# Kernel optimization log

Measured on AMD Instinct MI355X. Metric: run time of the kernel, lower is better.

The kernel has to match this reference:

```python
import jax, jax.numpy as jnp
from jax import lax
import numpy as np

L = 1024   # latent_size
R = 128    # latent_size // k
G = 2      # groups
KS = 2     # kernel_size
BI, BT, T, TXT = 32, 128, 64, 300
EPS = 1e-5


def setup_inputs() -> dict:
    key = jax.random.key(0)
    ks = jax.random.split(key, 24)
    n = lambda i, shape, s=0.05: jax.random.normal(ks[i], shape, jnp.float32) * s
    return {
        "img_embed": jax.random.normal(ks[0], (BI, 36, L), jnp.float32),
        "cap_embed": jax.random.normal(ks[1], (BT, T, TXT), jnp.float32),
        # reduce_img / reduce_txt (1x1 conv == linear over channels)
        "W_ri": n(2, (R, L)), "b_ri": n(3, (R,)),
        "W_rt": n(4, (R, TXT)), "b_rt": n(5, (R,)),
        # two MixedConv blocks stacked on a leading axis of size 2
        "mk_W": n(6, (2, R * R * KS // G, R)), "mk_b": n(7, (2, R * R * KS // G)),  # hypernet kernel Linear
        "mbias_W": n(8, (2, R, R)), "mbias_b": n(9, (2, R)),                        # hypernet bias Linear
        "wn_g": 1.0 + n(10, (2, R), 0.1), "wn_b": n(11, (2, R), 0.1),               # BN over generated kernel
        "ca_W": n(12, (2, R, R // G, KS)), "ca_b": n(13, (2, R)),                   # static grouped conv1a
        "bn_g": 1.0 + n(14, (2, 2 * R), 0.1), "bn_b": n(15, (2, 2 * R), 0.1),       # BN on cat activations
        "c1_W": n(16, (2, R, 2 * R)), "c1_b": n(17, (2, R)),                        # 1x1 mixing conv
        # txt_fc 1x1 conv
        "W_fc": n(18, (L, R)), "b_fc": n(19, (L,)),
    }


def _bn(x, g, b):
    # training-mode BatchNorm1d over (N, C, L): stats per channel over (N, L)
    m = x.mean(axis=(0, 2), keepdims=True)
    v = x.var(axis=(0, 2), keepdims=True)
    return g[None, :, None] * (x - m) * lax.rsqrt(v + EPS) + b[None, :, None]


def _gconv(x, w):
    # grouped valid conv1d, x: (B, Cin, T), w: (Cout, Cin//G, KS)
    return lax.conv_general_dilated(x, w, (1,), 'VALID',
                                    feature_group_count=G,
                                    dimension_numbers=('NCH', 'OIH', 'NCH'))


def _l2norm(x, axis=-1):
    return x / jnp.linalg.norm(x, axis=axis, keepdims=True)


def reference(img_embed, cap_embed, W_ri, b_ri, W_rt, b_rt, mk_W, mk_b,
              mbias_W, mbias_b, wn_g, wn_b, ca_W, ca_b, bn_g, bn_b,
              c1_W, c1_b, W_fc, b_fc):
    imgs = img_embed.transpose(0, 2, 1)   # (BI, L, 36)
    caps = cap_embed.transpose(0, 2, 1)   # (BT, 300, T)
    img_global = imgs.mean(-1)            # (BI, L)
    cap_red = jnp.einsum('oc,bct->bot', W_rt, caps) + b_rt[None, :, None]  # (BT, R, T)
    img_red = jnp.einsum('oc,bct->bot', W_ri, imgs) + b_ri[None, :, None]  # (BI, R, 36)
    img_vec = img_red.mean(-1)            # (BI, R) hypernet conditioning

    def mixed(x, base, j):
        # hypernet-generated grouped conv kernel + bias
        kern = (mk_W[j] @ base + mk_b[j]).reshape(R, R // G, KS)  # (out, in//g, ks)
        kern = _bn(kern.transpose(1, 0, 2), wn_g[j], wn_b[j]).transpose(1, 0, 2)
        bias = mbias_W[j] @ base + mbias_b[j]                     # (R,)
        px = _gconv(x, kern) + bias[None, :, None]
        ax = _gconv(x, ca_W[j]) + ca_b[j][None, :, None]
        h = jnp.concatenate([px, ax], axis=1)                     # (BT, 2R, T')
        h = jax.nn.relu(_bn(h, bn_g[j], bn_b[j]))
        return jnp.einsum('oc,bct->bot', c1_W[j], h) + c1_b[j][None, :, None]

    def per_image(base, img_g):
        x = mixed(cap_red, base, 0)
        x = mixed(x, base, 1)
        x = jnp.einsum('oc,bct->bot', W_fc, x) + b_fc[None, :, None]  # (BT, L, T-2)
        tv = _l2norm(jnp.max(x, axis=-1), axis=-1)                    # (BT, L)
        iv = _l2norm(img_g, axis=-1)                                  # (L,)
        return tv @ iv                                                # (BT,)

    sims = jax.vmap(per_image)(img_vec, img_global)  # (BI, BT)
    return sims
```

## Files before the change

### kernel.cpp

```cpp
#include <hip/hip_runtime.h>


#define EPSc 1e-5f
typedef unsigned short u16;
typedef __bf16 bf16x8 __attribute__((ext_vector_type(8)));
typedef float f32x4 __attribute__((ext_vector_type(4)));

static const long OFF_IMG_GLOBAL = 0;
static const long OFF_IV         = 32768;
static const long OFF_IMG_VEC    = 65536;
static const long OFF_CAP_RED    = 69632;
static const long OFF_KERN       = 1118208;
static const long OFF_KERN_BF    = 2166784;
static const long OFF_CA_BF      = 2691072;
static const long OFF_C1W0       = 2707456;
static const long OFF_C1W1       = 2715648;
static const long OFF_WFC        = 2732032;
static const long OFF_CAP_BF     = 2797568;
static const long OFF_SHARED1    = 3330112;
static const long OFF_ST_AX0     = 4378688;
static const long FIXED_END      = 4378944;

__device__ inline u16 f2bf(float f) {
  union { float f; unsigned u; } v; v.f = f;
  unsigned u = v.u;
  return (u16)((u + 0x7FFFu + ((u >> 16) & 1u)) >> 16);
}
__device__ inline float bf2f(u16 u) {
  union { unsigned u; float f; } v; v.u = ((unsigned)u) << 16; return v.f;
}

__global__ void k_img(const float* __restrict__ img, float* __restrict__ img_global,
                      float* __restrict__ iv) {
  int b = blockIdx.x, tid = threadIdx.x;
  __shared__ float gl[1024];
  __shared__ float red[256];
  float ssq = 0.f;
  for (int l = tid; l < 1024; l += 256) {
    float s = 0.f;
    for (int p = 0; p < 36; ++p) s += img[((long)b*36 + p)*1024 + l];
    float g = s * (1.f/36.f);
    gl[l] = g;
    img_global[(long)b*1024 + l] = g;
    ssq += g*g;
  }
  red[tid] = ssq;
  __syncthreads();
  for (int off = 128; off > 0; off >>= 1) {
    if (tid < off) red[tid] += red[tid+off];
    __syncthreads();
  }
  float inv = rsqrtf(red[0]);
  for (int l = tid; l < 1024; l += 256) iv[(long)b*1024 + l] = gl[l]*inv;
}

__global__ void k_imgvec(const float* __restrict__ img_global, const float* __restrict__ W_ri,
                         const float* __restrict__ b_ri, float* __restrict__ img_vec) {
  int b = blockIdx.x, tid = threadIdx.x;
  __shared__ float gl[1024];
  for (int l = tid; l < 1024; l += 128) gl[l] = img_global[(long)b*1024 + l];
  __syncthreads();
  const float* w = W_ri + (long)tid*1024;
  float acc = b_ri[tid];
  for (int l = 0; l < 1024; l += 4) {
    float4 wv = *(const float4*)(w + l);
    float4 gv = *(const float4*)(gl + l);
    acc += wv.x*gv.x + wv.y*gv.y + wv.z*gv.z + wv.w*gv.w;
  }
  img_vec[(long)b*128 + tid] = acc;
}

__global__ void k_capred(const float* __restrict__ cap, const float* __restrict__ W_rt,
                         const float* __restrict__ b_rt, float* __restrict__ cap_red) {
  int tg = blockIdx.x, b = blockIdx.y, tid = threadIdx.x;
  __shared__ float xs[300*16];
  for (int idx = tid; idx < 16*300; idx += 128) {
    int q = idx / 300, c = idx - q*300;
    xs[c*16 + q] = cap[((long)b*64 + tg*16 + q)*300 + c];
  }
  __syncthreads();
  int o = tid;
  const float* w = W_rt + (long)o*300;
  float acc[16];
  float bb = b_rt[o];
  #pragma unroll
  for (int q = 0; q < 16; ++q) acc[q] = bb;
  for (int c = 0; c < 300; ++c) {
    float wv = w[c];
    const float* xp = &xs[c*16];
    float4 x0 = *(const float4*)(xp);
    float4 x1 = *(const float4*)(xp+4);
    float4 x2 = *(const float4*)(xp+8);
    float4 x3 = *(const float4*)(xp+12);
    acc[0]+=wv*x0.x; acc[1]+=wv*x0.y; acc[2]+=wv*x0.z; acc[3]+=wv*x0.w;
    acc[4]+=wv*x1.x; acc[5]+=wv*x1.y; acc[6]+=wv*x1.z; acc[7]+=wv*x1.w;
    acc[8]+=wv*x2.x; acc[9]+=wv*x2.y; acc[10]+=wv*x2.z; acc[11]+=wv*x2.w;
    acc[12]+=wv*x3.x; acc[13]+=wv*x3.y; acc[14]+=wv*x3.z; acc[15]+=wv*x3.w;
  }
  float* outp = cap_red + ((long)b*128 + o)*64 + tg*16;
  #pragma unroll
  for (int q = 0; q < 16; ++q) outp[q] = acc[q];
}

__global__ void k_cap2bf(const float* __restrict__ cap_red, u16* __restrict__ cap_bf) {
  int b = blockIdx.x, tid = threadIdx.x;
  __shared__ float ls[128*64];
  for (int idx = tid; idx < 8192; idx += 256) ls[idx] = cap_red[(long)b*8192 + idx];
  __syncthreads();
  for (int idx = tid; idx < 65*128; idx += 256) {
    int t = idx >> 7, c = idx & 127;
    float v = (t < 64) ? ls[c*64 + t] : 0.f;
    cap_bf[((long)b*65 + t)*128 + c] = f2bf(v);
  }
}

__global__ void k_kerngen(const float* __restrict__ mk_W, const float* __restrict__ mk_b,
                          const float* __restrict__ img_vec, float* __restrict__ kern) {
  int j = blockIdx.x >> 7, kb = blockIdx.x & 127, tid = threadIdx.x;
  int k = kb*128 + tid;
  __shared__ float bl[128*32];
  for (int idx = tid; idx < 4096; idx += 128) {
    int i = idx >> 7, r = idx & 127;
    bl[r*32 + i] = img_vec[idx];
  }
  __syncthreads();
  const float* wrow = mk_W + ((long)j*16384 + k)*128;
  float acc[32];
  #pragma unroll
  for (int i = 0; i < 32; ++i) acc[i] = 0.f;
  for (int r = 0; r < 128; ++r) {
    float w = wrow[r];
    const float* bp = &bl[r*32];
    #pragma unroll
    for (int i = 0; i < 32; ++i) acc[i] += w * bp[i];
  }
  float kb_ = mk_b[(long)j*16384 + k];
  for (int i = 0; i < 32; ++i)
    kern[((long)j*32 + i)*16384 + k] = acc[i] + kb_;
}

__global__ void k_kernbn(const float* __restrict__ kern, const float* __restrict__ wn_g,
                         const float* __restrict__ wn_b, u16* __restrict__ kbf) {
  int j = blockIdx.x >> 5, i = blockIdx.x & 31, o = threadIdx.x;
  const float* row = kern + ((long)((j*32+i)*128 + o))*128;
  float s = 0.f, q = 0.f;
  for (int c = 0; c < 128; ++c) { float v = row[c]; s += v; q += v*v; }
  float mean = s * (1.f/128.f);
  float var = q * (1.f/128.f) - mean*mean;
  float rstd = rsqrtf(var + EPSc);
  float sc = wn_g[j*128+o] * rstd;
  float sh = wn_b[j*128+o] - mean*sc;
  int g = o >> 6, op = o & 63;
  u16* base = kbf + (((long)(j*32+i)*2 + g)*2)*4096 + op*64;
  for (int c = 0; c < 128; ++c) {
    float v = row[c]*sc + sh;
    int kp = c & 1, cp = c >> 1;
    base[(long)kp*4096 + cp] = f2bf(v);
  }
}

__global__ void k_ca2bf(const float* __restrict__ caW, u16* __restrict__ cabf) {
  int idx = blockIdx.x*256 + threadIdx.x;
  int j = idx >> 14, r = idx & 16383;
  int o = r >> 7, ck = r & 127, cp = ck >> 1, kp = ck & 1;
  int g = o >> 6, op = o & 63;
  cabf[(((long)(j*2+g)*2 + kp))*4096 + op*64 + cp] = f2bf(caW[idx]);
}

__global__ void k_c1bf(const float* __restrict__ c1W, u16* __restrict__ w0, u16* __restrict__ w1) {
  int idx = blockIdx.x*256 + threadIdx.x;
  if (idx < 16384) { int o = idx >> 7, c = idx & 127; w0[idx] = f2bf(c1W[o*256 + c]); }
  else { int e = idx - 16384; w1[e] = f2bf(c1W[32768 + e]); }
}

__global__ void k_wfc2bf(const float* __restrict__ W, u16* __restrict__ out) {
  int idx = (blockIdx.x*256 + threadIdx.x)*4;
  float4 v = *(const float4*)(W + idx);
  u16 o[4] = { f2bf(v.x), f2bf(v.y), f2bf(v.z), f2bf(v.w) };
  *(uint2*)(out + idx) = *(const uint2*)(o);
}

__global__ void k_conv(const float* __restrict__ X, long xstr, int Tin, int Tout,
                       const float* __restrict__ Wt, long wstr,
                       const float* __restrict__ bias, int bstr,
                       float* __restrict__ Y, long ystr) {
  int b = blockIdx.x, ic = blockIdx.y, tid = threadIdx.x;
  __shared__ float xls[128*64];
  const float* Xb = X + (long)ic*xstr + (long)b*128*Tin;
  for (int idx = tid; idx < 128*Tin; idx += 256) {
    int c = idx / Tin, t = idx - c*Tin;
    xls[c*64 + t] = Xb[idx];
  }
  __syncthreads();
  int oi = tid & 63, tq = tid >> 6;
  int o0 = oi*2, g = o0 >> 6, t0 = tq*16;
  const float* wa = Wt + (long)ic*wstr + (long)o0*128;
  const float* wb = wa + 128;
  float acc0[16], acc1[16];
  #pragma unroll
  for (int tt = 0; tt < 16; ++tt) { acc0[tt] = 0.f; acc1[tt] = 0.f; }
  bool f16ok = (t0 + 16 < Tin);
  for (int cp = 0; cp < 64; ++cp) {
    float wa0 = wa[cp*2], wa1 = wa[cp*2+1];
    float wb0 = wb[cp*2], wb1 = wb[cp*2+1];
    const float* row = &xls[(g*64 + cp)*64 + t0];
    float f[17];
    float4 v0 = *(const float4*)(row);
    float4 v1 = *(const float4*)(row+4);
    float4 v2 = *(const float4*)(row+8);
    float4 v3 = *(const float4*)(row+12);
    f[0]=v0.x; f[1]=v0.y; f[2]=v0.z; f[3]=v0.w;
    f[4]=v1.x; f[5]=v1.y; f[6]=v1.z; f[7]=v1.w;
    f[8]=v2.x; f[9]=v2.y; f[10]=v2.z; f[11]=v2.w;
    f[12]=v3.x; f[13]=v3.y; f[14]=v3.z; f[15]=v3.w;
    f[16] = f16ok ? row[16] : 0.f;
    #pragma unroll
    for (int tt = 0; tt < 16; ++tt) {
      acc0[tt] += wa0*f[tt] + wa1*f[tt+1];
      acc1[tt] += wb0*f[tt] + wb1*f[tt+1];
    }
  }
  float bb0 = bias[ic*bstr + o0], bb1 = bias[ic*bstr + o0 + 1];
  float* y0 = Y + (long)ic*ystr + ((long)b*128 + o0)*Tout;
  float* y1 = y0 + Tout;
  #pragma unroll
  for (int tt = 0; tt < 16; ++tt) {
    int t = t0 + tt;
    if (t < Tout) { y0[t] = acc0[tt] + bb0; y1[t] = acc1[tt] + bb1; }
  }
}

__global__ void k_stats(const float* __restrict__ X, long xstr, int Tlen,
                        const float* __restrict__ gp, const float* __restrict__ bp,
                        float* __restrict__ st, int sstr) {
  int c = blockIdx.x, ic = blockIdx.y, tid = threadIdx.x;
  __shared__ float r1[256], r2[256];
  const float* base = X + (long)ic*xstr + (long)c*Tlen;
  int n = 128*Tlen;
  float s = 0.f, q = 0.f;
  for (int idx = tid; idx < n; idx += 256) {
    int b = idx / Tlen, t = idx - b*Tlen;
    float v = base[(long)b*128*Tlen + t];
    s += v; q += v*v;
  }
  r1[tid] = s; r2[tid] = q;
  __syncthreads();
  for (int off = 128; off > 0; off >>= 1) {
    if (tid < off) { r1[tid] += r1[tid+off]; r2[tid] += r2[tid+off]; }
    __syncthreads();
  }
  if (tid == 0) {
    float mean = r1[0] / n;
    float var = r2[0] / n - mean*mean;
    float rstd = rsqrtf(var + EPSc);
    float sc = gp[c]*rstd;
    st[(long)ic*sstr + c] = sc;
    st[(long)ic*sstr + 128 + c] = bp[c] - mean*sc;
  }
}

__global__ void k_mix_shared(const float* __restrict__ X1, const float* __restrict__ st,
                             const float* __restrict__ W, float* __restrict__ Y) {
  int b = blockIdx.x, tid = threadIdx.x;
  __shared__ float xs[128*64];
  __shared__ float ssc[128], ssh[128];
  int o4 = (tid & 31)*4, t0 = (tid >> 5)*8;
  float acc[4][8];
  #pragma unroll
  for (int r = 0; r < 4; ++r)
    #pragma unroll
    for (int tt = 0; tt < 8; ++tt) acc[r][tt] = 0.f;
  if (tid < 128) { ssc[tid] = st[tid]; ssh[tid] = st[128+tid]; }
  __syncthreads();
  const float* Xb = X1 + (long)b*128*63;
  for (int idx = tid; idx < 128*63; idx += 256) {
    int c = idx / 63, t = idx - c*63;
    xs[c*64 + t] = fmaxf(Xb[idx]*ssc[c] + ssh[c], 0.f);
  }
  __syncthreads();
  for (int c = 0; c < 128; ++c) {
    float4 f0 = *(const float4*)&xs[c*64 + t0];
    float4 f1 = *(const float4*)&xs[c*64 + t0 + 4];
    #pragma unroll
    for (int r = 0; r < 4; ++r) {
      float w = W[(long)(o4+r)*256 + 128 + c];
      acc[r][0] += w*f0.x; acc[r][1] += w*f0.y; acc[r][2] += w*f0.z; acc[r][3] += w*f0.w;
      acc[r][4] += w*f1.x; acc[r][5] += w*f1.y; acc[r][6] += w*f1.z; acc[r][7] += w*f1.w;
    }
  }
  #pragma unroll
  for (int r = 0; r < 4; ++r)
    #pragma unroll
    for (int tt = 0; tt < 8; ++tt) {
      int t = t0 + tt;
      if (t < 63) Y[((long)b*64 + t)*128 + o4 + r] = acc[r][tt];
    }
}

__global__ __launch_bounds__(256) void k_conv_mfma2(
    const u16* __restrict__ X, long x_img_str, int tr_stride,
    const u16* __restrict__ kernA, const u16* __restrict__ statA,
    int tvalid, u16* __restrict__ H, int ctot, float* __restrict__ part) {
  int bc = blockIdx.x, v = blockIdx.y, i = blockIdx.z;
  int tid = threadIdx.x, w = tid >> 6, lane = tid & 63;
  int l15 = lane & 15, l4 = lane >> 4;
  int g = v & 1;
  const u16* A = (v >= 2) ? (statA + (long)g*8192)
                          : (kernA + (long)i*16384 + (long)g*8192);
  __shared__ u16 xls[65*64];
  bf16x8 af[2][2];
  #pragma unroll
  for (int kp = 0; kp < 2; ++kp)
    #pragma unroll
    for (int ks = 0; ks < 2; ++ks)
      af[kp][ks] = *(const bf16x8*)(A + ((long)(kp*64 + w*16 + l15))*64 + ks*32 + l4*8);
  int cbase = v*64 + w*16;
  float s[4] = {0.f,0.f,0.f,0.f}, q[4] = {0.f,0.f,0.f,0.f};
  for (int bb = 0; bb < 4; ++bb) {
    int b = bc*4 + bb;
    const u16* src = X + x_img_str*i + ((long)b*tr_stride)*128 + g*64;
    __syncthreads();
    for (int idx = tid; idx < 65*8; idx += 256) {
      int r = idx >> 3, ch = idx & 7;
      uint4 d = *(const uint4*)(src + (long)r*128 + ch*8);
      *(uint4*)(xls + r*64 + ((ch ^ (r & 7))*8)) = d;
    }
    __syncthreads();
    #pragma unroll
    for (int nt = 0; nt < 4; ++nt) {
      f32x4 acc = {0.f,0.f,0.f,0.f};
      #pragma unroll
      for (int kp = 0; kp < 2; ++kp) {
        int row = nt*16 + l15 + kp;
        #pragma unroll
        for (int ks = 0; ks < 2; ++ks) {
          int ch = (ks*4 + l4) ^ (row & 7);
          bf16x8 bf = *(const bf16x8*)(xls + row*64 + ch*8);
          acc = __builtin_amdgcn_mfma_f32_16x16x32_bf16(af[kp][ks], bf, acc, 0, 0, 0);
        }
      }
      int t = nt*16 + l15;
      u16 h4[4] = { f2bf(acc[0]), f2bf(acc[1]), f2bf(acc[2]), f2bf(acc[3]) };
      *(uint2*)(H + ((long)((i*128 + b)*64 + t))*ctot + cbase + l4*4) = *(const uint2*)(h4);
      float m = (t < tvalid) ? 1.f : 0.f;
      #pragma unroll
      for (int r = 0; r < 4; ++r) {
        float vv = acc[r]*m;
        s[r] += vv; q[r] += vv*vv;
      }
    }
  }
  #pragma unroll
  for (int r = 0; r < 4; ++r) {
    #pragma unroll
    for (int mk = 1; mk < 16; mk <<= 1) {
      s[r] += __shfl_xor(s[r], mk);
      q[r] += __shfl_xor(q[r], mk);
    }
  }
  if (l15 == 0) {
    #pragma unroll
    for (int r = 0; r < 4; ++r) {
      int c = cbase + l4*4 + r;
      long base = ((long)i*ctot + c)*64;
      part[base + bc] = s[r];
      part[base + 32 + bc] = q[r];
    }
  }
}

__global__ void k_finstats2(const float* __restrict__ part, float* __restrict__ scsh,
                            const float* __restrict__ g, const float* __restrict__ bta,
                            int ct, float n, int total) {
  int idx = blockIdx.x*256 + threadIdx.x;
  if (idx >= total) return;
  int c = idx & (ct - 1);
  const float* p = part + (long)idx*64;
  float s = 0.f, q = 0.f;
  #pragma unroll
  for (int k = 0; k < 32; ++k) { s += p[k]; q += p[32+k]; }
  float mean = s / n, var = q / n - mean*mean;
  float sc = g[c] * rsqrtf(var + EPSc);
  scsh[idx*2] = sc;
  scsh[idx*2 + 1] = bta[c] - mean*sc;
}

template<int CK>
__global__ __launch_bounds__(256) void k_mix_mfma2(
    const u16* __restrict__ X, const u16* __restrict__ A,
    const float* __restrict__ scsh,
    const float* __restrict__ c1b, const float* __restrict__ addbuf,
    u16* __restrict__ Q, int tvalid) {
  constexpr int NCH = CK/8;
  constexpr int KST = CK/32;
  int bc = blockIdx.x, m = blockIdx.y, i = blockIdx.z;
  int tid = threadIdx.x, w = tid >> 6, lane = tid & 63;
  int l15 = lane & 15, l4 = lane >> 4;
  __shared__ u16 xls[64*CK];
  __shared__ float lsc[CK], lsh[CK];
  for (int c = tid; c < CK; c += 256) {
    lsc[c] = scsh[((long)i*CK + c)*2];
    lsh[c] = scsh[((long)i*CK + c)*2 + 1];
  }
  int oa = m*64 + w*16 + l15;
  bf16x8 af[KST];
  #pragma unroll
  for (int ks = 0; ks < KST; ++ks)
    af[ks] = *(const bf16x8*)(A + (long)oa*CK + ks*32 + l4*8);
  int ob = m*64 + w*16 + l4*4;
  float4 cb;
  cb.x = c1b[ob]; cb.y = c1b[ob+1]; cb.z = c1b[ob+2]; cb.w = c1b[ob+3];
  for (int bb = 0; bb < 4; ++bb) {
    int b = bc*4 + bb;
    const u16* src = X + ((long)(i*128 + b)*64)*CK;
    __syncthreads();
    for (int idx = tid; idx < 64*NCH; idx += 256) {
      int r = idx / NCH, ch = idx & (NCH - 1);
      uint4 d = *(const uint4*)(src + (long)r*CK + ch*8);
      unsigned dd[4] = {d.x, d.y, d.z, d.w};
      int c0 = ch*8;
      u16 o[8];
      #pragma unroll
      for (int pi = 0; pi < 4; ++pi) {
        float v0 = bf2f((u16)(dd[pi] & 0xFFFF));
        float v1 = bf2f((u16)(dd[pi] >> 16));
        v0 = fmaxf(v0*lsc[c0 + pi*2] + lsh[c0 + pi*2], 0.f);
        v1 = fmaxf(v1*lsc[c0 + pi*2 + 1] + lsh[c0 + pi*2 + 1], 0.f);
        o[pi*2] = f2bf(v0); o[pi*2 + 1] = f2bf(v1);
      }
      *(uint4*)(xls + r*CK + (((ch ^ (r & 15)) & (NCH - 1))*8)) = *(const uint4*)o;
    }
    __syncthreads();
    #pragma unroll
    for (int nt = 0; nt < 4; ++nt) {
      f32x4 acc = {0.f,0.f,0.f,0.f};
      int row = nt*16 + l15;
      #pragma unroll
      for (int ks = 0; ks < KST; ++ks) {
        int ch = ((ks*4 + l4) ^ (row & 15)) & (NCH - 1);
        bf16x8 bf = *(const bf16x8*)(xls + row*CK + ch*8);
        acc = __builtin_amdgcn_mfma_f32_16x16x32_bf16(af[ks], bf, acc, 0, 0, 0);
      }
      int t = row;
      if (t < tvalid) {
        float4 ad = {0.f,0.f,0.f,0.f};
        if (addbuf) ad = *(const float4*)(addbuf + ((long)b*64 + t)*128 + ob);
        u16 h4[4] = { f2bf(acc[0] + cb.x + ad.x), f2bf(acc[1] + cb.y + ad.y),
                      f2bf(acc[2] + cb.z + ad.z), f2bf(acc[3] + cb.w + ad.w) };
        *(uint2*)(Q + ((long)((i*128 + b)*64 + t))*128 + ob) = *(const uint2*)(h4);
      }
    }
  }
}

__global__ __launch_bounds__(256) void k_fc3(
    const u16* __restrict__ Qt, const u16* __restrict__ Wb,
    const float* __restrict__ bfc, const float* __restrict__ ivp,
    float* __restrict__ pp) {
  int bg = blockIdx.x, sl = blockIdx.y, i = blockIdx.z;
  int tid = threadIdx.x, w = tid >> 6, lane = tid & 63;
  int l15 = lane & 15, l4 = lane >> 4;
  int lbase = sl*256 + w*64;
  bf16x8 wf[4][4];
  #pragma unroll
  for (int lt = 0; lt < 4; ++lt)
    #pragma unroll
    for (int ks = 0; ks < 4; ++ks)
      wf[lt][ks] = *(const bf16x8*)(Wb + (long)(lbase + lt*16 + l15)*128 + ks*32 + l4*8);
  float bfr[4], ivr[4];
  const float* ivb = ivp + (long)i*1024;
  #pragma unroll
  for (int lt = 0; lt < 4; ++lt) {
    bfr[lt] = bfc[lbase + lt*16 + l15];
    ivr[lt] = ivb[lbase + lt*16 + l15];
  }
  __shared__ float red[4][2];
  float en = (l4 == 0) ? 1.f : 0.f;
  for (int bb = 0; bb < 8; ++bb) {
    int b = bg*8 + bb;
    const u16* Qb = Qt + ((long)(i*128 + b))*64*128;
    float mx[4] = {-3e38f, -3e38f, -3e38f, -3e38f};
    #pragma unroll
    for (int nt = 0; nt < 4; ++nt) {
      bf16x8 qf[4];
      #pragma unroll
      for (int ks = 0; ks < 4; ++ks)
        qf[ks] = *(const bf16x8*)(Qb + (nt*16 + l15)*128 + ks*32 + l4*8);
      #pragma unroll
      for (int lt = 0; lt < 4; ++lt) {
        f32x4 acc = {0.f,0.f,0.f,0.f};
        acc = __builtin_amdgcn_mfma_f32_16x16x32_bf16(qf[0], wf[lt][0], acc, 0,0,0);
        acc = __builtin_amdgcn_mfma_f32_16x16x32_bf16(qf[1], wf[lt][1], acc, 0,0,0);
        acc = __builtin_amdgcn_mfma_f32_16x16x32_bf16(qf[2], wf[lt][2], acc, 0,0,0);
        acc = __builtin_amdgcn_mfma_f32_16x16x32_bf16(qf[3], wf[lt][3], acc, 0,0,0);
        float m01 = fmaxf(acc[0], acc[1]);
        float m23 = fmaxf(acc[2], acc[3]);
        if (nt == 3 && l4 == 3) m23 = -3e38f;
        mx[lt] = fmaxf(mx[lt], fmaxf(m01, m23));
      }
    }
    float ssc = 0.f, ddc = 0.f;
    #pragma unroll
    for (int lt = 0; lt < 4; ++lt) {
      float m = mx[lt];
      m = fmaxf(m, __shfl_xor(m, 16));
      m = fmaxf(m, __shfl_xor(m, 32));
      float tv = m + bfr[lt];
      ssc += en*tv*tv;
      ddc += en*tv*ivr[lt];
    }
    #pragma unroll
    for (int mk = 1; mk < 16; mk <<= 1) { ssc += __shfl_xor(ssc, mk); ddc += __shfl_xor(ddc, mk); }
    if (lane == 0) { red[w][0] = ssc; red[w][1] = ddc; }
    __syncthreads();
    if (tid == 0) {
      float S = red[0][0] + red[1][0] + red[2][0] + red[3][0];
      float D = red[0][1] + red[1][1] + red[2][1] + red[3][1];
      long o = (((long)i*128 + b)*4 + sl)*2;
      pp[o] = S; pp[o+1] = D;
    }
    __syncthreads();
  }
}

__global__ void k_fcred(const float* __restrict__ pp, float* __restrict__ outp) {
  int i = blockIdx.x, b = threadIdx.x;
  const float* p = pp + (((long)i*128 + b)*4)*2;
  float S = p[0] + p[2] + p[4] + p[6];
  float D = p[1] + p[3] + p[5] + p[7];
  outp[i*128 + b] = D * rsqrtf(S);
}

extern "C" void kernel_launch(void* const* d_in, const int* in_sizes, int n_in,
                              void* d_out, int out_size, void* d_ws, size_t ws_size,
                              hipStream_t stream) {
  (void)in_sizes; (void)n_in; (void)out_size;
  const float* img_embed = (const float*)d_in[0];
  const float* cap_embed = (const float*)d_in[1];
  const float* W_ri  = (const float*)d_in[2];
  const float* b_ri  = (const float*)d_in[3];
  const float* W_rt  = (const float*)d_in[4];
  const float* b_rt  = (const float*)d_in[5];
  const float* mk_W  = (const float*)d_in[6];
  const float* mk_b  = (const float*)d_in[7];
  const float* wn_g  = (const float*)d_in[10];
  const float* wn_b  = (const float*)d_in[11];
  const float* ca_W  = (const float*)d_in[12];
  const float* ca_b  = (const float*)d_in[13];
  const float* bn_g  = (const float*)d_in[14];
  const float* bn_b  = (const float*)d_in[15];
  const float* c1_W  = (const float*)d_in[16];
  const float* c1_b  = (const float*)d_in[17];
  const float* W_fc  = (const float*)d_in[18];
  const float* b_fc  = (const float*)d_in[19];
  float* out = (float*)d_out;
  float* ws  = (float*)d_ws;

  float* img_global = ws + OFF_IMG_GLOBAL;
  float* iv       = ws + OFF_IV;
  float* img_vec  = ws + OFF_IMG_VEC;
  float* cap_red  = ws + OFF_CAP_RED;
  float* kern     = ws + OFF_KERN;
  u16*   kern_bf  = (u16*)(ws + OFF_KERN_BF);
  u16*   ca_bf    = (u16*)(ws + OFF_CA_BF);
  u16*   c1w0     = (u16*)(ws + OFF_C1W0);
  u16*   c1w1     = (u16*)(ws + OFF_C1W1);
  u16*   wfcb     = (u16*)(ws + OFF_WFC);
  u16*   cap_bf   = (u16*)(ws + OFF_CAP_BF);
  float* shared1  = ws + OFF_SHARED1;
  float* st_ax0   = ws + OFF_ST_AX0;

  int NC = 4;
  {
    auto need = [](long nc) -> size_t { return (size_t)(FIXED_END + nc*2621440L + 128) * 4u; };
    if (ws_size >= need(32)) NC = 32;
    else if (ws_size >= need(16)) NC = 16;
    else if (ws_size >= need(8)) NC = 8;
  }

  float* part  = ws + OFF_KERN;
  float* scsh0 = ws + OFF_KERN + 524288;
  float* scsh1 = ws + OFF_KERN + 524288 + 8192;
  float* pp    = ws + OFF_KERN + 524288 + 8192 + 16384;

  long base = FIXED_END;
  float* ax0f = ws + base;
  u16* P0 = (u16*)(ws + base);
  u16* Q0 = (u16*)(ws + base + (long)NC*524288);
  u16* H1 = (u16*)(ws + base + (long)NC*524288*2 + 64);
  u16* Q1 = (u16*)(ws + base + (long)NC*524288*2 + 64 + (long)NC*1048576);

  k_img<<<32, 256, 0, stream>>>(img_embed, img_global, iv);
  k_imgvec<<<32, 128, 0, stream>>>(img_global, W_ri, b_ri, img_vec);
  k_capred<<<dim3(4,128), 128, 0, stream>>>(cap_embed, W_rt, b_rt, cap_red);
  k_cap2bf<<<128, 256, 0, stream>>>(cap_red, cap_bf);
  k_kerngen<<<256, 128, 0, stream>>>(mk_W, mk_b, img_vec, kern);
  k_kernbn<<<64, 128, 0, stream>>>(kern, wn_g, wn_b, kern_bf);
  k_ca2bf<<<128, 256, 0, stream>>>(ca_W, ca_bf);
  k_c1bf<<<192, 256, 0, stream>>>(c1_W, c1w0, c1w1);
  k_wfc2bf<<<128, 256, 0, stream>>>(W_fc, wfcb);

  k_conv<<<dim3(128,1), 256, 0, stream>>>(cap_red, 0, 64, 63, ca_W, 0, ca_b, 0, ax0f, 0);
  k_stats<<<dim3(128,1), 256, 0, stream>>>(ax0f, 0, 63, bn_g+128, bn_b+128, st_ax0, 0);
  k_mix_shared<<<128, 256, 0, stream>>>(ax0f, st_ax0, c1_W, shared1);

  for (int ch = 0; ch < 32/NC; ++ch) {
    int i0 = ch*NC;
    k_conv_mfma2<<<dim3(32,2,NC), 256, 0, stream>>>(
        cap_bf, 0L, 65, kern_bf + (long)i0*16384, ca_bf, 63, P0, 128, part);
    k_finstats2<<<dim3((NC*128+255)/256), 256, 0, stream>>>(
        part, scsh0, bn_g, bn_b, 128, 8064.f, NC*128);
    k_mix_mfma2<128><<<dim3(32,2,NC), 256, 0, stream>>>(
        P0, c1w0, scsh0, c1_b, shared1, Q0, 63);
    k_conv_mfma2<<<dim3(32,4,NC), 256, 0, stream>>>(
        Q0, 1048576L, 64, kern_bf + (long)(32 + i0)*16384, ca_bf + 16384, 62, H1, 256, part);
    k_finstats2<<<dim3((NC*256+255)/256), 256, 0, stream>>>(
        part, scsh1, bn_g + 256, bn_b + 256, 256, 7936.f, NC*256);
    k_mix_mfma2<256><<<dim3(32,2,NC), 256, 0, stream>>>(
        H1, c1w1, scsh1, c1_b + 128, nullptr, Q1, 62);
    k_fc3<<<dim3(16,4,NC), 256, 0, stream>>>(
        Q1, wfcb, b_fc, iv + (long)i0*1024, pp);
    k_fcred<<<NC, 128, 0, stream>>>(pp, out + i0*128);
  }
}
```

Baseline: 649.6 us.

## Software-pipeline global loads in conv, mix and fc kernels with register prefetch

The conv and mix MFMA kernels now prefetch the next batch's tile into registers while computing the current one, then write it to shared memory after a barrier, so global latency overlaps with MFMA work. The fc kernel double-buffers Q fragments across four captions per block, doubling the grid. It drops the block-level shared reduction in favour of per-wave partial outputs, and the final reduction kernel now sums 16 partials instead of 4. The cost is higher register pressure from the staged tiles and fragments, and more partial-sum traffic.

Measured after the change: 717.9 us. 1.11x slower.

```diff
diff --git a/kernel.cpp b/kernel.cpp
--- a/kernel.cpp
+++ b/kernel.cpp
@@ -297,7 +297,7 @@
     }
 }
 
-__global__ __launch_bounds__(256) void k_conv_mfma2(
+__global__ __launch_bounds__(256) void k_conv_mfma3(
     const u16* __restrict__ X, long x_img_str, int tr_stride,
     const u16* __restrict__ kernA, const u16* __restrict__ statA,
     int tvalid, u16* __restrict__ H, int ctot, float* __restrict__ part) {
@@ -316,16 +316,27 @@
       af[kp][ks] = *(const bf16x8*)(A + ((long)(kp*64 + w*16 + l15))*64 + ks*32 + l4*8);
   int cbase = v*64 + w*16;
   float s[4] = {0.f,0.f,0.f,0.f}, q[4] = {0.f,0.f,0.f,0.f};
+  uint4 s0, s1, s2;
+  int r0 = tid >> 3, ch0 = tid & 7;
+  int r1 = (tid + 256) >> 3, ch1 = tid & 7;
+  auto loadX = [&](int b) {
+    const u16* src = X + x_img_str*i + ((long)b*tr_stride)*128 + g*64;
+    s0 = *(const uint4*)(src + (long)r0*128 + ch0*8);
+    s1 = *(const uint4*)(src + (long)r1*128 + ch1*8);
+    if (tid < 8) s2 = *(const uint4*)(src + 64L*128 + tid*8);
+  };
+  auto writeX = [&]() {
+    *(uint4*)(xls + r0*64 + ((ch0 ^ (r0 & 7))*8)) = s0;
+    *(uint4*)(xls + r1*64 + ((ch1 ^ (r1 & 7))*8)) = s1;
+    if (tid < 8) *(uint4*)(xls + 64*64 + tid*8) = s2;
+  };
+  loadX(bc*4);
+  writeX();
+  __syncthreads();
+  #pragma unroll
   for (int bb = 0; bb < 4; ++bb) {
     int b = bc*4 + bb;
-    const u16* src = X + x_img_str*i + ((long)b*tr_stride)*128 + g*64;
-    __syncthreads();
-    for (int idx = tid; idx < 65*8; idx += 256) {
-      int r = idx >> 3, ch = idx & 7;
-      uint4 d = *(const uint4*)(src + (long)r*128 + ch*8);
-      *(uint4*)(xls + r*64 + ((ch ^ (r & 7))*8)) = d;
-    }
-    __syncthreads();
+    if (bb < 3) loadX(b + 1);
     #pragma unroll
     for (int nt = 0; nt < 4; ++nt) {
       f32x4 acc = {0.f,0.f,0.f,0.f};
@@ -349,6 +360,8 @@
         s[r] += vv; q[r] += vv*vv;
       }
     }
+    __syncthreads();
+    if (bb < 3) { writeX(); __syncthreads(); }
   }
   #pragma unroll
   for (int r = 0; r < 4; ++r) {
@@ -386,13 +399,14 @@
 }
 
 template<int CK>
-__global__ __launch_bounds__(256) void k_mix_mfma2(
+__global__ __launch_bounds__(256) void k_mix_mfma3(
     const u16* __restrict__ X, const u16* __restrict__ A,
     const float* __restrict__ scsh,
     const float* __restrict__ c1b, const float* __restrict__ addbuf,
     u16* __restrict__ Q, int tvalid) {
   constexpr int NCH = CK/8;
   constexpr int KST = CK/32;
+  constexpr int NST = (64*NCH)/256;
   int bc = blockIdx.x, m = blockIdx.y, i = blockIdx.z;
   int tid = threadIdx.x, w = tid >> 6, lane = tid & 63;
   int l15 = lane & 15, l4 = lane >> 4;
@@ -410,14 +424,21 @@
   int ob = m*64 + w*16 + l4*4;
   float4 cb;
   cb.x = c1b[ob]; cb.y = c1b[ob+1]; cb.z = c1b[ob+2]; cb.w = c1b[ob+3];
-  for (int bb = 0; bb < 4; ++bb) {
-    int b = bc*4 + bb;
+  uint4 st[NST];
+  auto loadX = [&](int b) {
     const u16* src = X + ((long)(i*128 + b)*64)*CK;
-    __syncthreads();
-    for (int idx = tid; idx < 64*NCH; idx += 256) {
+    #pragma unroll
+    for (int k = 0; k < NST; ++k) {
+      int idx = tid + k*256;
+      st[k] = *(const uint4*)(src + (long)(idx/NCH)*CK + (idx & (NCH-1))*8);
+    }
+  };
+  auto writeX = [&]() {
+    #pragma unroll
+    for (int k = 0; k < NST; ++k) {
+      int idx = tid + k*256;
       int r = idx / NCH, ch = idx & (NCH - 1);
-      uint4 d = *(const uint4*)(src + (long)r*CK + ch*8);
-      unsigned dd[4] = {d.x, d.y, d.z, d.w};
+      unsigned dd[4] = {st[k].x, st[k].y, st[k].z, st[k].w};
       int c0 = ch*8;
       u16 o[8];
       #pragma unroll
@@ -430,7 +451,15 @@
       }
       *(uint4*)(xls + r*CK + (((ch ^ (r & 15)) & (NCH - 1))*8)) = *(const uint4*)o;
     }
-    __syncthreads();
+  };
+  loadX(bc*4);
+  __syncthreads();
+  writeX();
+  __syncthreads();
+  #pragma unroll
+  for (int bb = 0; bb < 4; ++bb) {
+    int b = bc*4 + bb;
+    if (bb < 3) loadX(b + 1);
     #pragma unroll
     for (int nt = 0; nt < 4; ++nt) {
       f32x4 acc = {0.f,0.f,0.f,0.f};
@@ -450,10 +479,12 @@
         *(uint2*)(Q + ((long)((i*128 + b)*64 + t))*128 + ob) = *(const uint2*)(h4);
       }
     }
-  }
-}
-
-__global__ __launch_bounds__(256) void k_fc3(
+    __syncthreads();
+    if (bb < 3) { writeX(); __syncthreads(); }
+  }
+}
+
+__global__ __launch_bounds__(256) void k_fc4(
     const u16* __restrict__ Qt, const u16* __restrict__ Wb,
     const float* __restrict__ bfc, const float* __restrict__ ivp,
     float* __restrict__ pp) {
@@ -474,25 +505,26 @@
     bfr[lt] = bfc[lbase + lt*16 + l15];
     ivr[lt] = ivb[lbase + lt*16 + l15];
   }
-  __shared__ float red[4][2];
-  float en = (l4 == 0) ? 1.f : 0.f;
-  for (int bb = 0; bb < 8; ++bb) {
-    int b = bg*8 + bb;
-    const u16* Qb = Qt + ((long)(i*128 + b))*64*128;
-    float mx[4] = {-3e38f, -3e38f, -3e38f, -3e38f};
-    #pragma unroll
-    for (int nt = 0; nt < 4; ++nt) {
-      bf16x8 qf[4];
+  bf16x8 qA[4][4], qB[4][4];
+  auto loadQ = [&](bf16x8 (&qf)[4][4], int b) {
+    const u16* Qb = Qt + ((long)(i*128 + b))*8192;
+    #pragma unroll
+    for (int nt = 0; nt < 4; ++nt)
       #pragma unroll
       for (int ks = 0; ks < 4; ++ks)
-        qf[ks] = *(const bf16x8*)(Qb + (nt*16 + l15)*128 + ks*32 + l4*8);
+        qf[nt][ks] = *(const bf16x8*)(Qb + (nt*16 + l15)*128 + ks*32 + l4*8);
+  };
+  auto computeQ = [&](bf16x8 (&qf)[4][4], int b) {
+    float mx[4] = {-3e38f, -3e38f, -3e38f, -3e38f};
+    #pragma unroll
+    for (int nt = 0; nt < 4; ++nt) {
       #pragma unroll
       for (int lt = 0; lt < 4; ++lt) {
         f32x4 acc = {0.f,0.f,0.f,0.f};
-        acc = __builtin_amdgcn_mfma_f32_16x16x32_bf16(qf[0], wf[lt][0], acc, 0,0,0);
-        acc = __builtin_amdgcn_mfma_f32_16x16x32_bf16(qf[1], wf[lt][1], acc, 0,0,0);
-        acc = __builtin_amdgcn_mfma_f32_16x16x32_bf16(qf[2], wf[lt][2], acc, 0,0,0);
-        acc = __builtin_amdgcn_mfma_f32_16x16x32_bf16(qf[3], wf[lt][3], acc, 0,0,0);
+        acc = __builtin_amdgcn_mfma_f32_16x16x32_bf16(qf[nt][0], wf[lt][0], acc, 0,0,0);
+        acc = __builtin_amdgcn_mfma_f32_16x16x32_bf16(qf[nt][1], wf[lt][1], acc, 0,0,0);
+        acc = __builtin_amdgcn_mfma_f32_16x16x32_bf16(qf[nt][2], wf[lt][2], acc, 0,0,0);
+        acc = __builtin_amdgcn_mfma_f32_16x16x32_bf16(qf[nt][3], wf[lt][3], acc, 0,0,0);
         float m01 = fmaxf(acc[0], acc[1]);
         float m23 = fmaxf(acc[2], acc[3]);
         if (nt == 3 && l4 == 3) m23 = -3e38f;
@@ -506,28 +538,33 @@
       m = fmaxf(m, __shfl_xor(m, 16));
       m = fmaxf(m, __shfl_xor(m, 32));
       float tv = m + bfr[lt];
-      ssc += en*tv*tv;
-      ddc += en*tv*ivr[lt];
+      ssc += tv*tv;
+      ddc += tv*ivr[lt];
     }
     #pragma unroll
     for (int mk = 1; mk < 16; mk <<= 1) { ssc += __shfl_xor(ssc, mk); ddc += __shfl_xor(ddc, mk); }
-    if (lane == 0) { red[w][0] = ssc; red[w][1] = ddc; }
-    __syncthreads();
-    if (tid == 0) {
-      float S = red[0][0] + red[1][0] + red[2][0] + red[3][0];
-      float D = red[0][1] + red[1][1] + red[2][1] + red[3][1];
-      long o = (((long)i*128 + b)*4 + sl)*2;
-      pp[o] = S; pp[o+1] = D;
-    }
-    __syncthreads();
-  }
+    if (lane == 0) {
+      long o = (((long)i*128 + b)*16 + sl*4 + w)*2;
+      pp[o] = ssc; pp[o+1] = ddc;
+    }
+  };
+  int b0 = bg*4;
+  loadQ(qA, b0);
+  loadQ(qB, b0 + 1);
+  computeQ(qA, b0);
+  loadQ(qA, b0 + 2);
+  computeQ(qB, b0 + 1);
+  loadQ(qB, b0 + 3);
+  computeQ(qA, b0 + 2);
+  computeQ(qB, b0 + 3);
 }
 
 __global__ void k_fcred(const float* __restrict__ pp, float* __restrict__ outp) {
   int i = blockIdx.x, b = threadIdx.x;
-  const float* p = pp + (((long)i*128 + b)*4)*2;
-  float S = p[0] + p[2] + p[4] + p[6];
-  float D = p[1] + p[3] + p[5] + p[7];
+  const float* p = pp + ((long)i*128 + b)*32;
+  float S = 0.f, D = 0.f;
+  #pragma unroll
+  for (int k = 0; k < 16; ++k) { S += p[k*2]; D += p[k*2+1]; }
   outp[i*128 + b] = D * rsqrtf(S);
 }
 
@@ -606,19 +643,19 @@
 
   for (int ch = 0; ch < 32/NC; ++ch) {
     int i0 = ch*NC;
-    k_conv_mfma2<<<dim3(32,2,NC), 256, 0, stream>>>(
+    k_conv_mfma3<<<dim3(32,2,NC), 256, 0, stream>>>(
         cap_bf, 0L, 65, kern_bf + (long)i0*16384, ca_bf, 63, P0, 128, part);
     k_finstats2<<<dim3((NC*128+255)/256), 256, 0, stream>>>(
         part, scsh0, bn_g, bn_b, 128, 8064.f, NC*128);
-    k_mix_mfma2<128><<<dim3(32,2,NC), 256, 0, stream>>>(
+    k_mix_mfma3<128><<<dim3(32,2,NC), 256, 0, stream>>>(
         P0, c1w0, scsh0, c1_b, shared1, Q0, 63);
-    k_conv_mfma2<<<dim3(32,4,NC), 256, 0, stream>>>(
+    k_conv_mfma3<<<dim3(32,4,NC), 256, 0, stream>>>(
         Q0, 1048576L, 64, kern_bf + (long)(32 + i0)*16384, ca_bf + 16384, 62, H1, 256, part);
     k_finstats2<<<dim3((NC*256+255)/256), 256, 0, stream>>>(
         part, scsh1, bn_g + 256, bn_b + 256, 256, 7936.f, NC*256);
-    k_mix_mfma2<256><<<dim3(32,2,NC), 256, 0, stream>>>(
+    k_mix_mfma3<256><<<dim3(32,2,NC), 256, 0, stream>>>(
         H1, c1w1, scsh1, c1_b + 128, nullptr, Q1, 62);
-    k_fc3<<<dim3(16,4,NC), 256, 0, stream>>>(
+    k_fc4<<<dim3(32,4,NC), 256, 0, stream>>>(
         Q1, wfcb, b_fc, iv + (long)i0*1024, pp);
     k_fcred<<<NC, 128, 0, stream>>>(pp, out + i0*128);
   }
```

## Fuse kernel gen with BN, move shared ax path to MFMA, drop fc block syncs

Applied to the files above, without the earlier changes.

Merges hypernet kernel generation and its per-channel normalization into one kernel that keeps the generated values in shared memory, removing a global fp32 round trip and a launch. The image-independent static-conv branch (conv, stats, mixing) now reuses the existing bf16 MFMA conv/finstats/mix kernels instead of scalar fp32 kernels, with a new fp32-output template path and a split c1 weight buffer. The fc kernel drops its per-batch block-level reduction and syncthreads, writing per-wave partials that the final reduction sums over 16 entries. The static branch now runs in bf16, which can change numerics slightly.

After: 606.2 us. 6.7% less time.

```diff
diff --git a/kernel.cpp b/kernel.cpp
--- a/kernel.cpp
+++ b/kernel.cpp
@@ -13,13 +13,14 @@
 static const long OFF_KERN       = 1118208;
 static const long OFF_KERN_BF    = 2166784;
 static const long OFF_CA_BF      = 2691072;
-static const long OFF_C1W0       = 2707456;
-static const long OFF_C1W1       = 2715648;
-static const long OFF_WFC        = 2732032;
-static const long OFF_CAP_BF     = 2797568;
-static const long OFF_SHARED1    = 3330112;
-static const long OFF_ST_AX0     = 4378688;
-static const long FIXED_END      = 4378944;
+static const long OFF_C1W0      = 2707456;
+static const long OFF_C1W0X     = 2715648;
+static const long OFF_C1W1      = 2723840;
+static const long OFF_WFC       = 2740224;
+static const long OFF_CAP_BF    = 2805760;
+static const long OFF_SHARED1   = 3338304;
+static const long OFF_SCSHS     = 4386880;
+static const long FIXED_END     = 4387136;
 
 __device__ inline u16 f2bf(float f) {
   union { float f; unsigned u; } v; v.f = f;
@@ -114,17 +115,19 @@
   }
 }
 
-__global__ void k_kerngen(const float* __restrict__ mk_W, const float* __restrict__ mk_b,
-                          const float* __restrict__ img_vec, float* __restrict__ kern) {
-  int j = blockIdx.x >> 7, kb = blockIdx.x & 127, tid = threadIdx.x;
-  int k = kb*128 + tid;
+__global__ void k_kerngen2(const float* __restrict__ mk_W, const float* __restrict__ mk_b,
+                           const float* __restrict__ wn_g, const float* __restrict__ wn_b,
+                           const float* __restrict__ img_vec, u16* __restrict__ kbf) {
+  int j = blockIdx.x >> 7, o = blockIdx.x & 127, c = threadIdx.x;
   __shared__ float bl[128*32];
-  for (int idx = tid; idx < 4096; idx += 128) {
+  __shared__ float ls[128*33];
+  __shared__ float ssc[32], ssh[32];
+  for (int idx = c; idx < 4096; idx += 128) {
     int i = idx >> 7, r = idx & 127;
     bl[r*32 + i] = img_vec[idx];
   }
   __syncthreads();
-  const float* wrow = mk_W + ((long)j*16384 + k)*128;
+  const float* wrow = mk_W + ((long)(j*16384 + o*128 + c))*128;
   float acc[32];
   #pragma unroll
   for (int i = 0; i < 32; ++i) acc[i] = 0.f;
@@ -134,28 +137,25 @@
     #pragma unroll
     for (int i = 0; i < 32; ++i) acc[i] += w * bp[i];
   }
-  float kb_ = mk_b[(long)j*16384 + k];
-  for (int i = 0; i < 32; ++i)
-    kern[((long)j*32 + i)*16384 + k] = acc[i] + kb_;
-}
-
-__global__ void k_kernbn(const float* __restrict__ kern, const float* __restrict__ wn_g,
-                         const float* __restrict__ wn_b, u16* __restrict__ kbf) {
-  int j = blockIdx.x >> 5, i = blockIdx.x & 31, o = threadIdx.x;
-  const float* row = kern + ((long)((j*32+i)*128 + o))*128;
-  float s = 0.f, q = 0.f;
-  for (int c = 0; c < 128; ++c) { float v = row[c]; s += v; q += v*v; }
-  float mean = s * (1.f/128.f);
-  float var = q * (1.f/128.f) - mean*mean;
-  float rstd = rsqrtf(var + EPSc);
-  float sc = wn_g[j*128+o] * rstd;
-  float sh = wn_b[j*128+o] - mean*sc;
-  int g = o >> 6, op = o & 63;
-  u16* base = kbf + (((long)(j*32+i)*2 + g)*2)*4096 + op*64;
-  for (int c = 0; c < 128; ++c) {
-    float v = row[c]*sc + sh;
-    int kp = c & 1, cp = c >> 1;
-    base[(long)kp*4096 + cp] = f2bf(v);
+  float kb_ = mk_b[j*16384 + o*128 + c];
+  #pragma unroll
+  for (int i = 0; i < 32; ++i) ls[c*33 + i] = acc[i] + kb_;
+  __syncthreads();
+  if (c < 32) {
+    int i = c;
+    float s = 0.f, q = 0.f;
+    for (int cc = 0; cc < 128; ++cc) { float v = ls[cc*33 + i]; s += v; q += v*v; }
+    float mean = s * (1.f/128.f);
+    float var = q * (1.f/128.f) - mean*mean;
+    float sc = wn_g[j*128+o] * rsqrtf(var + EPSc);
+    ssc[i] = sc;
+    ssh[i] = wn_b[j*128+o] - mean*sc;
+  }
+  __syncthreads();
+  int g = o >> 6, op = o & 63, kp = c & 1, cp = c >> 1;
+  for (int i = 0; i < 32; ++i) {
+    float v = ls[c*33 + i]*ssc[i] + ssh[i];
+    kbf[((long)((j*32+i)*2 + g)*2 + kp)*4096 + op*64 + cp] = f2bf(v);
   }
 }
 
@@ -167,10 +167,16 @@
   cabf[(((long)(j*2+g)*2 + kp))*4096 + op*64 + cp] = f2bf(caW[idx]);
 }
 
-__global__ void k_c1bf(const float* __restrict__ c1W, u16* __restrict__ w0, u16* __restrict__ w1) {
+__global__ void k_c1bf(const float* __restrict__ c1W, u16* __restrict__ w0a,
+                       u16* __restrict__ w0x, u16* __restrict__ w1) {
   int idx = blockIdx.x*256 + threadIdx.x;
-  if (idx < 16384) { int o = idx >> 7, c = idx & 127; w0[idx] = f2bf(c1W[o*256 + c]); }
-  else { int e = idx - 16384; w1[e] = f2bf(c1W[32768 + e]); }
+  u16 v = f2bf(c1W[idx]);
+  if (idx < 32768) {
+    int o = idx >> 8, c = idx & 255;
+    if (c < 128) w0a[o*128 + c] = v; else w0x[o*128 + (c-128)] = v;
+  } else {
+    w1[idx - 32768] = v;
+  }
 }
 
 __global__ void k_wfc2bf(const float* __restrict__ W, u16* __restrict__ out) {
@@ -178,123 +184,6 @@
   float4 v = *(const float4*)(W + idx);
   u16 o[4] = { f2bf(v.x), f2bf(v.y), f2bf(v.z), f2bf(v.w) };
   *(uint2*)(out + idx) = *(const uint2*)(o);
-}
-
-__global__ void k_conv(const float* __restrict__ X, long xstr, int Tin, int Tout,
-                       const float* __restrict__ Wt, long wstr,
-                       const float* __restrict__ bias, int bstr,
-                       float* __restrict__ Y, long ystr) {
-  int b = blockIdx.x, ic = blockIdx.y, tid = threadIdx.x;
-  __shared__ float xls[128*64];
-  const float* Xb = X + (long)ic*xstr + (long)b*128*Tin;
-  for (int idx = tid; idx < 128*Tin; idx += 256) {
-    int c = idx / Tin, t = idx - c*Tin;
-    xls[c*64 + t] = Xb[idx];
-  }
-  __syncthreads();
-  int oi = tid & 63, tq = tid >> 6;
-  int o0 = oi*2, g = o0 >> 6, t0 = tq*16;
-  const float* wa = Wt + (long)ic*wstr + (long)o0*128;
-  const float* wb = wa + 128;
-  float acc0[16], acc1[16];
-  #pragma unroll
-  for (int tt = 0; tt < 16; ++tt) { acc0[tt] = 0.f; acc1[tt] = 0.f; }
-  bool f16ok = (t0 + 16 < Tin);
-  for (int cp = 0; cp < 64; ++cp) {
-    float wa0 = wa[cp*2], wa1 = wa[cp*2+1];
-    float wb0 = wb[cp*2], wb1 = wb[cp*2+1];
-    const float* row = &xls[(g*64 + cp)*64 + t0];
-    float f[17];
-    float4 v0 = *(const float4*)(row);
-    float4 v1 = *(const float4*)(row+4);
-    float4 v2 = *(const float4*)(row+8);
-    float4 v3 = *(const float4*)(row+12);
-    f[0]=v0.x; f[1]=v0.y; f[2]=v0.z; f[3]=v0.w;
-    f[4]=v1.x; f[5]=v1.y; f[6]=v1.z; f[7]=v1.w;
-    f[8]=v2.x; f[9]=v2.y; f[10]=v2.z; f[11]=v2.w;
-    f[12]=v3.x; f[13]=v3.y; f[14]=v3.z; f[15]=v3.w;
-    f[16] = f16ok ? row[16] : 0.f;
-    #pragma unroll
-    for (int tt = 0; tt < 16; ++tt) {
-      acc0[tt] += wa0*f[tt] + wa1*f[tt+1];
-      acc1[tt] += wb0*f[tt] + wb1*f[tt+1];
-    }
-  }
-  float bb0 = bias[ic*bstr + o0], bb1 = bias[ic*bstr + o0 + 1];
-  float* y0 = Y + (long)ic*ystr + ((long)b*128 + o0)*Tout;
-  float* y1 = y0 + Tout;
-  #pragma unroll
-  for (int tt = 0; tt < 16; ++tt) {
-    int t = t0 + tt;
-    if (t < Tout) { y0[t] = acc0[tt] + bb0; y1[t] = acc1[tt] + bb1; }
-  }
-}
-
-__global__ void k_stats(const float* __restrict__ X, long xstr, int Tlen,
-                        const float* __restrict__ gp, const float* __restrict__ bp,
-                        float* __restrict__ st, int sstr) {
-  int c = blockIdx.x, ic = blockIdx.y, tid = threadIdx.x;
-  __shared__ float r1[256], r2[256];
-  const float* base = X + (long)ic*xstr + (long)c*Tlen;
-  int n = 128*Tlen;
-  float s = 0.f, q = 0.f;
-  for (int idx = tid; idx < n; idx += 256) {
-    int b = idx / Tlen, t = idx - b*Tlen;
-    float v = base[(long)b*128*Tlen + t];
-    s += v; q += v*v;
-  }
-  r1[tid] = s; r2[tid] = q;
-  __syncthreads();
-  for (int off = 128; off > 0; off >>= 1) {
-    if (tid < off) { r1[tid] += r1[tid+off]; r2[tid] += r2[tid+off]; }
-    __syncthreads();
-  }
-  if (tid == 0) {
-    float mean = r1[0] / n;
-    float var = r2[0] / n - mean*mean;
-    float rstd = rsqrtf(var + EPSc);
-    float sc = gp[c]*rstd;
-    st[(long)ic*sstr + c] = sc;
-    st[(long)ic*sstr + 128 + c] = bp[c] - mean*sc;
-  }
-}
-
-__global__ void k_mix_shared(const float* __restrict__ X1, const float* __restrict__ st,
-                             const float* __restrict__ W, float* __restrict__ Y) {
-  int b = blockIdx.x, tid = threadIdx.x;
-  __shared__ float xs[128*64];
-  __shared__ float ssc[128], ssh[128];
-  int o4 = (tid & 31)*4, t0 = (tid >> 5)*8;
-  float acc[4][8];
-  #pragma unroll
-  for (int r = 0; r < 4; ++r)
-    #pragma unroll
-    for (int tt = 0; tt < 8; ++tt) acc[r][tt] = 0.f;
-  if (tid < 128) { ssc[tid] = st[tid]; ssh[tid] = st[128+tid]; }
-  __syncthreads();
-  const float* Xb = X1 + (long)b*128*63;
-  for (int idx = tid; idx < 128*63; idx += 256) {
-    int c = idx / 63, t = idx - c*63;
-    xs[c*64 + t] = fmaxf(Xb[idx]*ssc[c] + ssh[c], 0.f);
-  }
-  __syncthreads();
-  for (int c = 0; c < 128; ++c) {
-    float4 f0 = *(const float4*)&xs[c*64 + t0];
-    float4 f1 = *(const float4*)&xs[c*64 + t0 + 4];
-    #pragma unroll
-    for (int r = 0; r < 4; ++r) {
-      float w = W[(long)(o4+r)*256 + 128 + c];
-      acc[r][0] += w*f0.x; acc[r][1] += w*f0.y; acc[r][2] += w*f0.z; acc[r][3] += w*f0.w;
-      acc[r][4] += w*f1.x; acc[r][5] += w*f1.y; acc[r][6] += w*f1.z; acc[r][7] += w*f1.w;
-    }
-  }
-  #pragma unroll
-  for (int r = 0; r < 4; ++r)
-    #pragma unroll
-    for (int tt = 0; tt < 8; ++tt) {
-      int t = t0 + tt;
-      if (t < 63) Y[((long)b*64 + t)*128 + o4 + r] = acc[r][tt];
-    }
 }
 
 __global__ __launch_bounds__(256) void k_conv_mfma2(
@@ -385,12 +274,12 @@
   scsh[idx*2 + 1] = bta[c] - mean*sc;
 }
 
-template<int CK>
+template<int CK, bool F32OUT>
 __global__ __launch_bounds__(256) void k_mix_mfma2(
     const u16* __restrict__ X, const u16* __restrict__ A,
     const float* __restrict__ scsh,
     const float* __restrict__ c1b, const float* __restrict__ addbuf,
-    u16* __restrict__ Q, int tvalid) {
+    void* __restrict__ Qout, int tvalid) {
   constexpr int NCH = CK/8;
   constexpr int KST = CK/32;
   int bc = blockIdx.x, m = blockIdx.y, i = blockIdx.z;
@@ -408,8 +297,8 @@
   for (int ks = 0; ks < KST; ++ks)
     af[ks] = *(const bf16x8*)(A + (long)oa*CK + ks*32 + l4*8);
   int ob = m*64 + w*16 + l4*4;
-  float4 cb;
-  cb.x = c1b[ob]; cb.y = c1b[ob+1]; cb.z = c1b[ob+2]; cb.w = c1b[ob+3];
+  float4 cb = {0.f,0.f,0.f,0.f};
+  if (c1b) { cb.x = c1b[ob]; cb.y = c1b[ob+1]; cb.z = c1b[ob+2]; cb.w = c1b[ob+3]; }
   for (int bb = 0; bb < 4; ++bb) {
     int b = bc*4 + bb;
     const u16* src = X + ((long)(i*128 + b)*64)*CK;
@@ -443,17 +332,22 @@
       }
       int t = row;
       if (t < tvalid) {
-        float4 ad = {0.f,0.f,0.f,0.f};
-        if (addbuf) ad = *(const float4*)(addbuf + ((long)b*64 + t)*128 + ob);
-        u16 h4[4] = { f2bf(acc[0] + cb.x + ad.x), f2bf(acc[1] + cb.y + ad.y),
-                      f2bf(acc[2] + cb.z + ad.z), f2bf(acc[3] + cb.w + ad.w) };
-        *(uint2*)(Q + ((long)((i*128 + b)*64 + t))*128 + ob) = *(const uint2*)(h4);
+        if constexpr (F32OUT) {
+          float4 o4 = { acc[0]+cb.x, acc[1]+cb.y, acc[2]+cb.z, acc[3]+cb.w };
+          *(float4*)((float*)Qout + ((long)((i*128 + b)*64 + t))*128 + ob) = o4;
+        } else {
+          float4 ad = {0.f,0.f,0.f,0.f};
+          if (addbuf) ad = *(const float4*)(addbuf + ((long)b*64 + t)*128 + ob);
+          u16 h4[4] = { f2bf(acc[0] + cb.x + ad.x), f2bf(acc[1] + cb.y + ad.y),
+                        f2bf(acc[2] + cb.z + ad.z), f2bf(acc[3] + cb.w + ad.w) };
+          *(uint2*)((u16*)Qout + ((long)((i*128 + b)*64 + t))*128 + ob) = *(const uint2*)(h4);
+        }
       }
     }
   }
 }
 
-__global__ __launch_bounds__(256) void k_fc3(
+__global__ __launch_bounds__(256) void k_fc5(
     const u16* __restrict__ Qt, const u16* __restrict__ Wb,
     const float* __restrict__ bfc, const float* __restrict__ ivp,
     float* __restrict__ pp) {
@@ -474,11 +368,9 @@
     bfr[lt] = bfc[lbase + lt*16 + l15];
     ivr[lt] = ivb[lbase + lt*16 + l15];
   }
-  __shared__ float red[4][2];
-  float en = (l4 == 0) ? 1.f : 0.f;
   for (int bb = 0; bb < 8; ++bb) {
     int b = bg*8 + bb;
-    const u16* Qb = Qt + ((long)(i*128 + b))*64*128;
+    const u16* Qb = Qt + ((long)(i*128 + b))*8192;
     float mx[4] = {-3e38f, -3e38f, -3e38f, -3e38f};
     #pragma unroll
     for (int nt = 0; nt < 4; ++nt) {
@@ -506,28 +398,24 @@
       m = fmaxf(m, __shfl_xor(m, 16));
       m = fmaxf(m, __shfl_xor(m, 32));
       float tv = m + bfr[lt];
-      ssc += en*tv*tv;
-      ddc += en*tv*ivr[lt];
+      ssc += tv*tv;
+      ddc += tv*ivr[lt];
     }
     #pragma unroll
     for (int mk = 1; mk < 16; mk <<= 1) { ssc += __shfl_xor(ssc, mk); ddc += __shfl_xor(ddc, mk); }
-    if (lane == 0) { red[w][0] = ssc; red[w][1] = ddc; }
-    __syncthreads();
-    if (tid == 0) {
-      float S = red[0][0] + red[1][0] + red[2][0] + red[3][0];
-      float D = red[0][1] + red[1][1] + red[2][1] + red[3][1];
-      long o = (((long)i*128 + b)*4 + sl)*2;
-      pp[o] = S; pp[o+1] = D;
-    }
-    __syncthreads();
+    if (lane == 0) {
+      long o = (((long)i*128 + b)*16 + sl*4 + w)*2;
+      pp[o] = ssc; pp[o+1] = ddc;
+    }
   }
 }
 
 __global__ void k_fcred(const float* __restrict__ pp, float* __restrict__ outp) {
   int i = blockIdx.x, b = threadIdx.x;
-  const float* p = pp + (((long)i*128 + b)*4)*2;
-  float S = p[0] + p[2] + p[4] + p[6];
-  float D = p[1] + p[3] + p[5] + p[7];
+  const float* p = pp + ((long)i*128 + b)*32;
+  float S = 0.f, D = 0.f;
+  #pragma unroll
+  for (int k = 0; k < 16; ++k) { S += p[k*2]; D += p[k*2+1]; }
   outp[i*128 + b] = D * rsqrtf(S);
 }
 
@@ -546,7 +434,6 @@
   const float* wn_g  = (const float*)d_in[10];
   const float* wn_b  = (const float*)d_in[11];
   const float* ca_W  = (const float*)d_in[12];
-  const float* ca_b  = (const float*)d_in[13];
   const float* bn_g  = (const float*)d_in[14];
   const float* bn_b  = (const float*)d_in[15];
   const float* c1_W  = (const float*)d_in[16];
@@ -560,15 +447,15 @@
   float* iv       = ws + OFF_IV;
   float* img_vec  = ws + OFF_IMG_VEC;
   float* cap_red  = ws + OFF_CAP_RED;
-  float* kern     = ws + OFF_KERN;
   u16*   kern_bf  = (u16*)(ws + OFF_KERN_BF);
   u16*   ca_bf    = (u16*)(ws + OFF_CA_BF);
-  u16*   c1w0     = (u16*)(ws + OFF_C1W0);
+  u16*   c1w0a    = (u16*)(ws + OFF_C1W0);
+  u16*   c1w0x    = (u16*)(ws + OFF_C1W0X);
   u16*   c1w1     = (u16*)(ws + OFF_C1W1);
   u16*   wfcb     = (u16*)(ws + OFF_WFC);
   u16*   cap_bf   = (u16*)(ws + OFF_CAP_BF);
   float* shared1  = ws + OFF_SHARED1;
-  float* st_ax0   = ws + OFF_ST_AX0;
+  float* scshS    = ws + OFF_SCSHS;
 
   int NC = 4;
   {
@@ -584,25 +471,26 @@
   float* pp    = ws + OFF_KERN + 524288 + 8192 + 16384;
 
   long base = FIXED_END;
-  float* ax0f = ws + base;
   u16* P0 = (u16*)(ws + base);
   u16* Q0 = (u16*)(ws + base + (long)NC*524288);
   u16* H1 = (u16*)(ws + base + (long)NC*524288*2 + 64);
   u16* Q1 = (u16*)(ws + base + (long)NC*524288*2 + 64 + (long)NC*1048576);
+  u16* ax0bf = P0;
 
   k_img<<<32, 256, 0, stream>>>(img_embed, img_global, iv);
   k_imgvec<<<32, 128, 0, stream>>>(img_global, W_ri, b_ri, img_vec);
   k_capred<<<dim3(4,128), 128, 0, stream>>>(cap_embed, W_rt, b_rt, cap_red);
   k_cap2bf<<<128, 256, 0, stream>>>(cap_red, cap_bf);
-  k_kerngen<<<256, 128, 0, stream>>>(mk_W, mk_b, img_vec, kern);
-  k_kernbn<<<64, 128, 0, stream>>>(kern, wn_g, wn_b, kern_bf);
+  k_kerngen2<<<256, 128, 0, stream>>>(mk_W, mk_b, wn_g, wn_b, img_vec, kern_bf);
   k_ca2bf<<<128, 256, 0, stream>>>(ca_W, ca_bf);
-  k_c1bf<<<192, 256, 0, stream>>>(c1_W, c1w0, c1w1);
+  k_c1bf<<<256, 256, 0, stream>>>(c1_W, c1w0a, c1w0x, c1w1);
   k_wfc2bf<<<128, 256, 0, stream>>>(W_fc, wfcb);
 
-  k_conv<<<dim3(128,1), 256, 0, stream>>>(cap_red, 0, 64, 63, ca_W, 0, ca_b, 0, ax0f, 0);
-  k_stats<<<dim3(128,1), 256, 0, stream>>>(ax0f, 0, 63, bn_g+128, bn_b+128, st_ax0, 0);
-  k_mix_shared<<<128, 256, 0, stream>>>(ax0f, st_ax0, c1_W, shared1);
+  k_conv_mfma2<<<dim3(32,2,1), 256, 0, stream>>>(
+      cap_bf, 0L, 65, ca_bf, ca_bf, 63, ax0bf, 128, part);
+  k_finstats2<<<1, 256, 0, stream>>>(part, scshS, bn_g + 128, bn_b + 128, 128, 8064.f, 128);
+  k_mix_mfma2<128, true><<<dim3(32,2,1), 256, 0, stream>>>(
+      ax0bf, c1w0x, scshS, nullptr, nullptr, shared1, 63);
 
   for (int ch = 0; ch < 32/NC; ++ch) {
     int i0 = ch*NC;
@@ -610,15 +498,15 @@
         cap_bf, 0L, 65, kern_bf + (long)i0*16384, ca_bf, 63, P0, 128, part);
     k_finstats2<<<dim3((NC*128+255)/256), 256, 0, stream>>>(
         part, scsh0, bn_g, bn_b, 128, 8064.f, NC*128);
-    k_mix_mfma2<128><<<dim3(32,2,NC), 256, 0, stream>>>(
-        P0, c1w0, scsh0, c1_b, shared1, Q0, 63);
+    k_mix_mfma2<128, false><<<dim3(32,2,NC), 256, 0, stream>>>(
+        P0, c1w0a, scsh0, c1_b, shared1, Q0, 63);
     k_conv_mfma2<<<dim3(32,4,NC), 256, 0, stream>>>(
         Q0, 1048576L, 64, kern_bf + (long)(32 + i0)*16384, ca_bf + 16384, 62, H1, 256, part);
     k_finstats2<<<dim3((NC*256+255)/256), 256, 0, stream>>>(
         part, scsh1, bn_g + 256, bn_b + 256, 256, 7936.f, NC*256);
-    k_mix_mfma2<256><<<dim3(32,2,NC), 256, 0, stream>>>(
+    k_mix_mfma2<256, false><<<dim3(32,2,NC), 256, 0, stream>>>(
         H1, c1w1, scsh1, c1_b + 128, nullptr, Q1, 62);
-    k_fc3<<<dim3(16,4,NC), 256, 0, stream>>>(
+    k_fc5<<<dim3(16,4,NC), 256, 0, stream>>>(
         Q1, wfcb, b_fc, iv + (long)i0*1024, pp);
     k_fcred<<<NC, 128, 0, stream>>>(pp, out + i0*128);
   }
```
